# Kernel optimization log

Hardware: AMD Instinct MI355X
Metric: run time of the kernel (lower is better)

The kernel has to match this reference:

```python
import jax, jax.numpy as jnp
import numpy as np

D_MODEL = 512
HEADS = 8
HEAD_DIM = D_MODEL // HEADS
LN_EPS = 1e-5


def _rel_shift(pos_score):
    # pos_score: [B, H, T, P] with P = 2T-1
    B, H, T, P = pos_score.shape
    padded = jnp.pad(pos_score, ((0, 0), (0, 0), (0, 0), (1, 0)))  # [B,H,T,P+1]
    shifted = padded.reshape(B, H, P + 1, T)[:, :, 1:, :].reshape(B, H, T, P)
    return shifted[:, :, :, : P // 2 + 1]  # [B,H,T,T]


def setup_inputs() -> dict:
    key = jax.random.key(0)
    ks = jax.random.split(key, 16)
    B, T = 16, 512
    P = 2 * T - 1
    s = 1.0 / np.sqrt(D_MODEL)
    inp = {
        "x": jax.random.normal(ks[0], (B, T, D_MODEL), jnp.float32),
        "pos_emb": jax.random.normal(ks[1], (B, P, D_MODEL), jnp.float32),
        "ln_g": jnp.ones((D_MODEL,), jnp.float32),
        "ln_b": jnp.zeros((D_MODEL,), jnp.float32),
        "Wq": jax.random.normal(ks[2], (D_MODEL, D_MODEL), jnp.float32) * s,
        "bq": jnp.zeros((D_MODEL,), jnp.float32),
        "Wk": jax.random.normal(ks[3], (D_MODEL, D_MODEL), jnp.float32) * s,
        "bk": jnp.zeros((D_MODEL,), jnp.float32),
        "Wv": jax.random.normal(ks[4], (D_MODEL, D_MODEL), jnp.float32) * s,
        "bv": jnp.zeros((D_MODEL,), jnp.float32),
        "Wp": jax.random.normal(ks[5], (D_MODEL, D_MODEL), jnp.float32) * s,
        "bp": jnp.zeros((D_MODEL,), jnp.float32),
        "content_bias": jax.random.normal(ks[6], (HEADS, HEAD_DIM), jnp.float32) * 0.05,
        "position_bias": jax.random.normal(ks[7], (HEADS, HEAD_DIM), jnp.float32) * 0.05,
        "Wo": jax.random.normal(ks[8], (D_MODEL, D_MODEL), jnp.float32) * s,
        "bo": jnp.zeros((D_MODEL,), jnp.float32),
    }
    return inp


def reference(x, pos_emb, ln_g, ln_b, Wq, bq, Wk, bk, Wv, bv, Wp, bp,
              content_bias, position_bias, Wo, bo):
    B, T, D = x.shape
    H, hd = HEADS, HEAD_DIM

    # LayerNorm over last dim
    mu = jnp.mean(x, axis=-1, keepdims=True)
    var = jnp.var(x, axis=-1, keepdims=True)
    xn = (x - mu) / jnp.sqrt(var + LN_EPS) * ln_g + ln_b

    q = (xn @ Wq.T + bq).reshape(B, T, H, hd)                 # [B,T,H,hd]
    k = (xn @ Wk.T + bk).reshape(B, T, H, hd)                 # [B,T,H,hd]
    v = (xn @ Wv.T + bv).reshape(B, T, H, hd)                 # [B,T,H,hd]
    p = (pos_emb @ Wp.T + bp).reshape(B, -1, H, hd)           # [B,P,H,hd]

    content_score = jnp.einsum('bshd,bthd->bhst', q + content_bias, k)   # [B,H,T,T]
    pos_score = jnp.einsum('bshd,bphd->bhsp', q + position_bias, p)      # [B,H,T,P]
    pos_score = _rel_shift(pos_score)                                    # [B,H,T,T]

    scores = (content_score + pos_score) / jnp.sqrt(jnp.asarray(hd, x.dtype))
    w = jax.nn.softmax(scores, axis=-1)
    ctx = jnp.einsum('bhst,bthd->bshd', w, v).reshape(B, T, D)
    return ctx @ Wo.T + bo
```

## Files before the change

kernel.cpp:

```cpp
#include <hip/hip_runtime.h>
#include <cstdio>
#include <cstdint>


typedef short s16x8 __attribute__((ext_vector_type(8)));
typedef float f32x4 __attribute__((ext_vector_type(4)));
typedef unsigned short u16x4 __attribute__((ext_vector_type(4)));

#define CSCALE 0.1803368801111204f

#if __has_builtin(__builtin_amdgcn_exp2f)
#define EXP2(x) __builtin_amdgcn_exp2f(x)
#else
#define EXP2(x) exp2f(x)
#endif

__device__ __forceinline__ unsigned short f2bf(float f) {
  unsigned int u = __builtin_bit_cast(unsigned int, f);
  unsigned int r = (u + 0x7FFFu + ((u >> 16) & 1u)) >> 16;
  return (unsigned short)r;
}
__device__ __forceinline__ float bf2f(unsigned short h) {
  unsigned int u = ((unsigned int)h) << 16;
  return __builtin_bit_cast(float, u);
}

__device__ __forceinline__ void g2l16(const void* g, void* l) {
  __builtin_amdgcn_global_load_lds(
      (const __attribute__((address_space(1))) void*)g,
      (__attribute__((address_space(3))) void*)l, 16, 0, 0);
}

__global__ __launch_bounds__(256) void megaprep(
    const float* __restrict__ x, const float* __restrict__ g,
    const float* __restrict__ bb, unsigned short* __restrict__ xh,
    const float* __restrict__ pe, unsigned short* __restrict__ ped,
    const float* __restrict__ Wq, const float* __restrict__ Wk,
    const float* __restrict__ Wp, const float* __restrict__ Wv,
    const float* __restrict__ Wo, const float* __restrict__ bq,
    const float* __restrict__ bk, unsigned short* __restrict__ wqk,
    unsigned short* __restrict__ wpm, unsigned short* __restrict__ wvm,
    unsigned short* __restrict__ wom, float* __restrict__ bqk) {
  __shared__ float red[8];
  const int bid = blockIdx.x, tid = threadIdx.x;
  if (bid < 8192) {
    const int wave = tid >> 6, lane = tid & 63;
    const float* xr = x + (size_t)bid * 512;
    float v0 = xr[tid], v1 = xr[tid + 256];
    float s = v0 + v1, ss = v0 * v0 + v1 * v1;
#pragma unroll
    for (int d = 1; d < 64; d <<= 1) {
      s += __shfl_xor(s, d, 64);
      ss += __shfl_xor(ss, d, 64);
    }
    if (lane == 0) { red[wave] = s; red[4 + wave] = ss; }
    __syncthreads();
    s = red[0] + red[1] + red[2] + red[3];
    ss = red[4] + red[5] + red[6] + red[7];
    const float mu = s * (1.0f / 512.0f);
    const float var = ss * (1.0f / 512.0f) - mu * mu;
    const float rstd = rsqrtf(var + 1e-5f);
#pragma unroll
    for (int i = 0; i < 2; i++) {
      int d = tid + i * 256;
      float v = (i == 0) ? v0 : v1;
      float xn = (v - mu) * rstd * g[d] + bb[d];
      xh[(size_t)bid * 512 + d] = f2bf(xn);
    }
  } else if (bid < 16384) {
    int e0 = (bid - 8192) * 1024 + tid * 4;
    u16x4 o = {0, 0, 0, 0};
    if (e0 < 16368 * 512) {
      float4 v = *(const float4*)(pe + e0);
      o[0] = f2bf(v.x); o[1] = f2bf(v.y); o[2] = f2bf(v.z); o[3] = f2bf(v.w);
    }
    *(u16x4*)(ped + e0) = o;
  } else {
    int idx = (bid - 16384) * 1024 + tid * 4;
    int region = idx >> 18, off = idx & 262143;
    const float* src = (region == 0)   ? Wq
                       : (region == 1) ? Wk
                       : (region == 2) ? Wp
                       : (region == 3) ? Wv
                                       : Wo;
    float4 w = *(const float4*)(src + off);
    u16x4 hv;
    hv[0] = f2bf(w.x); hv[1] = f2bf(w.y); hv[2] = f2bf(w.z); hv[3] = f2bf(w.w);
    unsigned short* dst = (region == 0)   ? wqk
                          : (region == 1) ? wqk + 262144
                          : (region == 2) ? wpm
                          : (region == 3) ? wvm
                                          : wom;
    *(u16x4*)(dst + off) = hv;
    if (idx < 1024) {
#pragma unroll
      for (int j = 0; j < 4; j++) {
        int ii = idx + j;
        bqk[ii] = (ii < 512) ? bq[ii] : bk[ii - 512];
      }
    }
  }
}

__device__ __forceinline__ void gemm128_body(
    unsigned short* sm, int mode, int arow0, int m0e, int n0,
    const unsigned short* __restrict__ A, const unsigned short* __restrict__ B,
    const float* __restrict__ bias, void* __restrict__ O1, void* __restrict__ O2,
    void* __restrict__ O3, const float* __restrict__ cbv,
    const float* __restrict__ pbv) {
  unsigned short* bA = sm;
  unsigned short* bB = sm + 4096;
  const int tid = threadIdx.x, lane = tid & 63, wave = tid >> 6;
  const int wr = (wave >> 1) * 64, wc = (wave & 1) * 64;
  const int fr = lane & 15, hi2 = lane >> 4;
  const int l15 = lane & 15, lq = lane >> 4;

  f32x4 fz = {0.f, 0.f, 0.f, 0.f};
  f32x4 acc[4][4];
#pragma unroll
  for (int i = 0; i < 4; i++)
#pragma unroll
    for (int j = 0; j < 4; j++) acc[i][j] = fz;

  const unsigned short* gA0 = A + (size_t)(arow0 + wave * 32 + l15) * 512 + lq * 8;
  const unsigned short* gA1 = gA0 + 16 * 512;
  const unsigned short* gB0 = B + (size_t)(n0 + wave * 32 + l15) * 512 + lq * 8;
  const unsigned short* gB1 = gB0 + 16 * 512;
  char* dA0 = (char*)bA + wave * 2048;
  char* dA1 = dA0 + 1024;
  char* dB0 = (char*)bB + wave * 2048;
  char* dB1 = dB0 + 1024;
  const int atile = 4 * (wave >> 1), btile = 4 * (wave & 1);

  for (int k0 = 0; k0 < 512; k0 += 32) {
    __syncthreads();
    g2l16(gA0 + k0, dA0);
    g2l16(gA1 + k0, dA1);
    g2l16(gB0 + k0, dB0);
    g2l16(gB1 + k0, dB1);
    __syncthreads();
    s16x8 af[4], bf[4];
#pragma unroll
    for (int mt = 0; mt < 4; ++mt)
      af[mt] = *(const s16x8*)&bA[(atile + mt) * 512 + lane * 8];
#pragma unroll
    for (int nt = 0; nt < 4; ++nt)
      bf[nt] = *(const s16x8*)&bB[(btile + nt) * 512 + lane * 8];
#pragma unroll
    for (int mt = 0; mt < 4; ++mt)
#pragma unroll
      for (int nt = 0; nt < 4; ++nt)
        acc[mt][nt] = __builtin_amdgcn_mfma_f32_16x16x32_bf16(
            af[mt], bf[nt], acc[mt][nt], 0, 0, 0);
  }
#pragma unroll
  for (int nt = 0; nt < 4; ++nt) {
    int col = n0 + wc + nt * 16 + fr;
    float bval = bias[col];
#pragma unroll
    for (int mt = 0; mt < 4; ++mt) {
      int rowb_l = wr + mt * 16 + hi2 * 4;
      if (mode == 0) {
#pragma unroll
        for (int r = 0; r < 4; ++r)
          ((float*)O1)[(size_t)(m0e + rowb_l + r) * 512 + col] =
              acc[mt][nt][r] + bval;
      } else if (mode == 1) {
        int b = m0e >> 10, u0 = m0e & 1023;
        int h = col >> 6, cc = col & 63;
        size_t cbase = (size_t)(b * 8 + h) * 64 * 1024 + (cc >> 5) * 512 +
                       ((cc & 31) >> 3) * 128 + (cc & 7);
#pragma unroll
        for (int r = 0; r < 4; ++r) {
          int u = u0 + rowb_l + r;
          float val = (u >= 1023) ? 0.f : (acc[mt][nt][r] + bval);
          ((unsigned short*)O1)[cbase + (size_t)(u >> 4) * 1024 + (u & 15) * 8] =
              f2bf(val);
        }
      } else if (mode == 2) {
        int row = m0e + rowb_l;
        int b = row >> 9, s15 = row & 15, s16i = (row & 511) >> 4;
        if (col < 512) {
          int h = col >> 6, cc = col & 63;
          size_t idx = ((size_t)(b * 8 + h) * 32 + s16i) * 1024 +
                       (cc >> 5) * 512 + ((cc & 31) >> 3) * 128 + (cc & 7);
#pragma unroll
          for (int r = 0; r < 4; ++r) {
            float val = acc[mt][nt][r] + bval;
            ((unsigned short*)O1)[idx + (s15 + r) * 8] =
                f2bf((val + cbv[col]) * CSCALE);
            ((unsigned short*)O2)[idx + (s15 + r) * 8] =
                f2bf((val + pbv[col]) * CSCALE);
          }
        } else {
          int c2 = col - 512, h = c2 >> 6, cc = c2 & 63;
          size_t idx = ((size_t)(b * 8 + h) * 32 + s16i) * 1024 +
                       (cc >> 5) * 512 + ((cc & 31) >> 3) * 128 + (cc & 7);
#pragma unroll
          for (int r = 0; r < 4; ++r)
            ((unsigned short*)O3)[idx + (s15 + r) * 8] =
                f2bf(acc[mt][nt][r] + bval);
        }
      } else {
        int rowb = m0e + rowb_l;
        int b = rowb >> 9, t = rowb & 511;
        int h = col >> 6, d = col & 63;
        size_t idx = ((size_t)((b * 8 + h) * 4 + (d >> 4)) * 16 + (t >> 5)) * 512 +
                     ((t & 31) >> 3) * 128 + (d & 15) * 8 + (t & 7);
        u16x4 hv;
#pragma unroll
        for (int r = 0; r < 4; ++r) hv[r] = f2bf(acc[mt][nt][r] + bval);
        *(u16x4*)((unsigned short*)O1 + idx) = hv;
      }
    }
  }
}

__global__ __launch_bounds__(256) void proj_all(
    const unsigned short* __restrict__ xn_hi, const unsigned short* __restrict__ pe_hi,
    const unsigned short* __restrict__ wqk, const unsigned short* __restrict__ wpm,
    const unsigned short* __restrict__ wvm, const float* __restrict__ bqk,
    const float* __restrict__ bp, const float* __restrict__ bv,
    const float* __restrict__ cbv, const float* __restrict__ pbv,
    unsigned short* __restrict__ qc, unsigned short* __restrict__ qp,
    unsigned short* __restrict__ kb, unsigned short* __restrict__ pbuf,
    unsigned short* __restrict__ vth) {
  __shared__ __align__(16) unsigned short sm[8192];
  const int id = blockIdx.x;
  if (id < 512) {
    int m0 = (id >> 3) * 128, n0 = (id & 7) * 128;
    gemm128_body(sm, 2, m0, m0, n0, xn_hi, wqk, bqk, qc, qp, kb, cbv, pbv);
  } else if (id < 1024) {
    int l = id - 512;
    int y = l >> 2, n0 = (l & 3) * 128;
    int b = y >> 3, mt8 = y & 7;
    gemm128_body(sm, 1, b * 1023 + mt8 * 128, b * 1024 + mt8 * 128, n0, pe_hi,
                 wpm, bp, pbuf, nullptr, nullptr, nullptr, nullptr);
  } else {
    int l = id - 1024;
    int m0 = (l >> 2) * 128, n0 = (l & 3) * 128;
    gemm128_body(sm, 3, m0, m0, n0, xn_hi, wvm, bv, vth, nullptr, nullptr,
                 nullptr, nullptr);
  }
}

__global__ __launch_bounds__(256) void out_gemm(
    const unsigned short* __restrict__ ctx, const unsigned short* __restrict__ wom,
    const float* __restrict__ bo, float* __restrict__ out) {
  __shared__ __align__(16) unsigned short sm[8192];
  const int id = blockIdx.x;
  int m0 = (id >> 2) * 128, n0 = (id & 3) * 128;
  gemm128_body(sm, 0, m0, m0, n0, ctx, wom, bo, out, nullptr, nullptr,
               nullptr, nullptr);
}

__global__ __launch_bounds__(256) void flash_attn(
    const unsigned short* __restrict__ qc, const unsigned short* __restrict__ qp,
    const unsigned short* __restrict__ kb, const unsigned short* __restrict__ pm,
    const unsigned short* __restrict__ vth, unsigned short* __restrict__ ctx) {
  const int id = blockIdx.x;
  const int bh = id & 127, b = bh >> 3, h = bh & 7;
  const int s_blk = id >> 7;
  const int tid = threadIdx.x, wave = tid >> 6, lane = tid & 63;
  const int fr = lane & 15, hi2 = lane >> 4, fc = hi2 * 8;
  const int s0w = s_blk * 64 + wave * 16;
  const int crow = hi2 * 4;

  __shared__ __align__(16) unsigned short Ph_s[4][16][40];
  unsigned short(*Phw)[40] = Ph_s[wave];

  int srcl[4];
#pragma unroll
  for (int r = 0; r < 4; ++r) srcl[r] = (hi2 << 4) | ((fr - (crow + r) - 1) & 15);

  const size_t qtb = ((size_t)(b * 8 + h) * 32 + (s0w >> 4)) * 1024 + lane * 8;
  s16x8 aqc0 = *(const s16x8*)(qc + qtb);
  s16x8 aqc1 = *(const s16x8*)(qc + qtb + 512);
  s16x8 aqp0 = *(const s16x8*)(qp + qtb);
  s16x8 aqp1 = *(const s16x8*)(qp + qtb + 512);

  const unsigned short* kpk = kb + (size_t)(b * 8 + h) * 32 * 1024 + lane * 8;
  const unsigned short* ppk = pm + (size_t)(b * 8 + h) * 64 * 1024 + lane * 8;
  const unsigned short* vhk = vth + (size_t)(b * 8 + h) * 64 * 512 + lane * 8;

  f32x4 fz = {0.f, 0.f, 0.f, 0.f};
  f32x4 Oacc[4] = {fz, fz, fz, fz};
  float lsum[4] = {0.f, 0.f, 0.f, 0.f};

  for (int step = 0; step < 16; ++step) {
    const int t0 = step * 32;
    const int u0w = t0 - s0w + 496;
    const int kt = t0 >> 4, ut = u0w >> 4, vt = t0 >> 5;
    f32x4 sc[2] = {fz, fz};
#pragma unroll
    for (int nt = 0; nt < 2; ++nt) {
      const unsigned short* kr = kpk + (size_t)(kt + nt) * 1024;
      s16x8 b0 = *(const s16x8*)kr;
      s16x8 b1 = *(const s16x8*)(kr + 512);
      sc[nt] = __builtin_amdgcn_mfma_f32_16x16x32_bf16(aqc0, b0, sc[nt], 0, 0, 0);
      sc[nt] = __builtin_amdgcn_mfma_f32_16x16x32_bf16(aqc1, b1, sc[nt], 0, 0, 0);
    }
    f32x4 sp[3];
#pragma unroll
    for (int nt = 0; nt < 3; ++nt) {
      const unsigned short* pr = ppk + (size_t)(ut + nt) * 1024;
      s16x8 b0 = *(const s16x8*)pr;
      s16x8 b1 = *(const s16x8*)(pr + 512);
      f32x4 t = fz;
      t = __builtin_amdgcn_mfma_f32_16x16x32_bf16(aqp0, b0, t, 0, 0, 0);
      t = __builtin_amdgcn_mfma_f32_16x16x32_bf16(aqp1, b1, t, 0, 0, 0);
      sp[nt] = t;
    }
    float sj[3][4];
#pragma unroll
    for (int j = 0; j < 3; ++j)
#pragma unroll
      for (int r = 0; r < 4; ++r) sj[j][r] = __shfl(sp[j][r], srcl[r], 64);
#pragma unroll
    for (int nt = 0; nt < 2; ++nt) {
      int tc = nt * 16 + fr;
#pragma unroll
      for (int r = 0; r < 4; ++r) {
        float pos = (fr <= crow + r) ? sj[nt][r] : sj[nt + 1][r];
        float e = EXP2(sc[nt][r] + pos);
        lsum[r] += e;
        Phw[crow + r][tc] = f2bf(e);
      }
    }
    s16x8 ah = *(const s16x8*)&Phw[fr][fc];
#pragma unroll
    for (int nt = 0; nt < 4; ++nt) {
      s16x8 bh = *(const s16x8*)(vhk + (size_t)(nt * 16 + vt) * 512);
      Oacc[nt] = __builtin_amdgcn_mfma_f32_16x16x32_bf16(ah, bh, Oacc[nt], 0, 0, 0);
    }
  }
#pragma unroll
  for (int d = 1; d < 16; d <<= 1)
#pragma unroll
    for (int r = 0; r < 4; ++r) lsum[r] += __shfl_xor(lsum[r], d, 64);
#pragma unroll
  for (int nt = 0; nt < 4; ++nt)
#pragma unroll
    for (int r = 0; r < 4; ++r) {
      float o = Oacc[nt][r] / lsum[r];
      size_t idx =
          (size_t)(b * 512 + s0w + crow + r) * 512 + h * 64 + nt * 16 + fr;
      ctx[idx] = f2bf(o);
    }
}

extern "C" void kernel_launch(void* const* d_in, const int* in_sizes, int n_in,
                              void* d_out, int out_size, void* d_ws,
                              size_t ws_size, hipStream_t stream) {
  const float* x = (const float*)d_in[0];
  const float* pe = (const float*)d_in[1];
  const float* ln_g = (const float*)d_in[2];
  const float* ln_b = (const float*)d_in[3];
  const float* Wq = (const float*)d_in[4];
  const float* bq = (const float*)d_in[5];
  const float* Wk = (const float*)d_in[6];
  const float* bk = (const float*)d_in[7];
  const float* Wv = (const float*)d_in[8];
  const float* bv = (const float*)d_in[9];
  const float* Wp = (const float*)d_in[10];
  const float* bp = (const float*)d_in[11];
  const float* cb = (const float*)d_in[12];
  const float* pb = (const float*)d_in[13];
  const float* Wo = (const float*)d_in[14];
  const float* bo = (const float*)d_in[15];
  float* out = (float*)d_out;

  char* ws = (char*)d_ws;
  size_t off = 0;
  auto alloc = [&](size_t bytes) -> char* {
    char* ptr = ws + off;
    off = (off + bytes + 255) & ~(size_t)255;
    return ptr;
  };
  unsigned short* xn_hi = (unsigned short*)alloc((size_t)8192 * 512 * 2);
  unsigned short* ctx = xn_hi;
  unsigned short* pe_hi = (unsigned short*)alloc((size_t)16384 * 512 * 2);
  unsigned short* vt_hi = (unsigned short*)alloc((size_t)8192 * 512 * 2);
  unsigned short* wqk = (unsigned short*)alloc((size_t)1024 * 512 * 2);
  unsigned short* wpm = (unsigned short*)alloc((size_t)512 * 512 * 2);
  unsigned short* wvm = (unsigned short*)alloc((size_t)512 * 512 * 2);
  unsigned short* wom = (unsigned short*)alloc((size_t)512 * 512 * 2);
  float* bqk = (float*)alloc(1024 * 4);
  unsigned short* qc = (unsigned short*)alloc((size_t)8192 * 512 * 2);
  unsigned short* qp = (unsigned short*)alloc((size_t)8192 * 512 * 2);
  unsigned short* kbuf = (unsigned short*)alloc((size_t)8192 * 512 * 2);
  unsigned short* pbuf = (unsigned short*)alloc((size_t)16384 * 512 * 2);

  if (ws_size < off) {
    fprintf(stderr, "kernel_launch: ws too small (need %zu, have %zu)\n", off,
            ws_size);
    return;
  }

  megaprep<<<17664, 256, 0, stream>>>(x, ln_g, ln_b, xn_hi, pe, pe_hi, Wq, Wk,
                                      Wp, Wv, Wo, bq, bk, wqk, wpm, wvm, wom,
                                      bqk);
  proj_all<<<1280, 256, 0, stream>>>(xn_hi, pe_hi, wqk, wpm, wvm, bqk, bp, bv,
                                     cb, pb, qc, qp, kbuf, pbuf, vt_hi);
  flash_attn<<<1024, 256, 0, stream>>>(qc, qp, kbuf, pbuf, vt_hi, ctx);
  out_gemm<<<256, 256, 0, stream>>>(ctx, wom, bo, out);
}
```

Before: 232.9 us.

## Pre-pack GEMM operands into MFMA fragment layout and load directly without LDS

The prep kernel and attention output now write activations, positional embeddings and weights in a packed 16-row by 32-col fragment layout. This lets the projection and output GEMMs load MFMA operands straight from global memory per wave, with no LDS staging and no block barriers. Tiles shrink from 128x128 per block to 64x64 per wave. This removes shared-memory round trips and syncs, but gives up operand reuse across waves, so global and L2 traffic rises and the scattered packed writes in prep add cost.

```diff
diff --git a/kernel.cpp b/kernel.cpp
--- a/kernel.cpp
+++ b/kernel.cpp
@@ -24,17 +24,15 @@
   unsigned int u = ((unsigned int)h) << 16;
   return __builtin_bit_cast(float, u);
 }
-
-__device__ __forceinline__ void g2l16(const void* g, void* l) {
-  __builtin_amdgcn_global_load_lds(
-      (const __attribute__((address_space(1))) void*)g,
-      (__attribute__((address_space(3))) void*)l, 16, 0, 0);
+__device__ __forceinline__ size_t pk(int row, int col) {
+  return (size_t)(row >> 4) * 8192 + (col >> 5) * 512 + ((col >> 3) & 3) * 128 +
+         (row & 15) * 8 + (col & 7);
 }
 
 __global__ __launch_bounds__(256) void megaprep(
     const float* __restrict__ x, const float* __restrict__ g,
-    const float* __restrict__ bb, unsigned short* __restrict__ xh,
-    const float* __restrict__ pe, unsigned short* __restrict__ ped,
+    const float* __restrict__ bb, unsigned short* __restrict__ xpk,
+    const float* __restrict__ pe, unsigned short* __restrict__ pepk,
     const float* __restrict__ Wq, const float* __restrict__ Wk,
     const float* __restrict__ Wp, const float* __restrict__ Wv,
     const float* __restrict__ Wo, const float* __restrict__ bq,
@@ -65,16 +63,18 @@
       int d = tid + i * 256;
       float v = (i == 0) ? v0 : v1;
       float xn = (v - mu) * rstd * g[d] + bb[d];
-      xh[(size_t)bid * 512 + d] = f2bf(xn);
+      xpk[pk(bid, d)] = f2bf(xn);
     }
   } else if (bid < 16384) {
-    int e0 = (bid - 8192) * 1024 + tid * 4;
+    int e = (bid - 8192) * 1024 + tid * 4;
+    int r = e >> 9, c = e & 511;
+    int b = r >> 10, u = r & 1023;
     u16x4 o = {0, 0, 0, 0};
-    if (e0 < 16368 * 512) {
-      float4 v = *(const float4*)(pe + e0);
+    if (u < 1023) {
+      float4 v = *(const float4*)(pe + (size_t)(b * 1023 + u) * 512 + c);
       o[0] = f2bf(v.x); o[1] = f2bf(v.y); o[2] = f2bf(v.z); o[3] = f2bf(v.w);
     }
-    *(u16x4*)(ped + e0) = o;
+    *(u16x4*)(pepk + (size_t)b * 524288 + pk(u, c)) = o;
   } else {
     int idx = (bid - 16384) * 1024 + tid * 4;
     int region = idx >> 18, off = idx & 262143;
@@ -86,12 +86,15 @@
     float4 w = *(const float4*)(src + off);
     u16x4 hv;
     hv[0] = f2bf(w.x); hv[1] = f2bf(w.y); hv[2] = f2bf(w.z); hv[3] = f2bf(w.w);
-    unsigned short* dst = (region == 0)   ? wqk
-                          : (region == 1) ? wqk + 262144
-                          : (region == 2) ? wpm
-                          : (region == 3) ? wvm
-                                          : wom;
-    *(u16x4*)(dst + off) = hv;
+    int n = off >> 9, k = off & 511;
+    unsigned short* dst;
+    int nrow = n;
+    if (region == 0) { dst = wqk; }
+    else if (region == 1) { dst = wqk; nrow = n + 512; }
+    else if (region == 2) { dst = wpm; }
+    else if (region == 3) { dst = wvm; }
+    else { dst = wom; }
+    *(u16x4*)(dst + pk(nrow, k)) = hv;
     if (idx < 1024) {
 #pragma unroll
       for (int j = 0; j < 4; j++) {
@@ -102,50 +105,20 @@
   }
 }
 
-__device__ __forceinline__ void gemm128_body(
-    unsigned short* sm, int mode, int arow0, int m0e, int n0,
-    const unsigned short* __restrict__ A, const unsigned short* __restrict__ B,
-    const float* __restrict__ bias, void* __restrict__ O1, void* __restrict__ O2,
-    void* __restrict__ O3, const float* __restrict__ cbv,
-    const float* __restrict__ pbv) {
-  unsigned short* bA = sm;
-  unsigned short* bB = sm + 4096;
-  const int tid = threadIdx.x, lane = tid & 63, wave = tid >> 6;
-  const int wr = (wave >> 1) * 64, wc = (wave & 1) * 64;
-  const int fr = lane & 15, hi2 = lane >> 4;
-  const int l15 = lane & 15, lq = lane >> 4;
-
-  f32x4 fz = {0.f, 0.f, 0.f, 0.f};
-  f32x4 acc[4][4];
-#pragma unroll
-  for (int i = 0; i < 4; i++)
-#pragma unroll
-    for (int j = 0; j < 4; j++) acc[i][j] = fz;
-
-  const unsigned short* gA0 = A + (size_t)(arow0 + wave * 32 + l15) * 512 + lq * 8;
-  const unsigned short* gA1 = gA0 + 16 * 512;
-  const unsigned short* gB0 = B + (size_t)(n0 + wave * 32 + l15) * 512 + lq * 8;
-  const unsigned short* gB1 = gB0 + 16 * 512;
-  char* dA0 = (char*)bA + wave * 2048;
-  char* dA1 = dA0 + 1024;
-  char* dB0 = (char*)bB + wave * 2048;
-  char* dB1 = dB0 + 1024;
-  const int atile = 4 * (wave >> 1), btile = 4 * (wave & 1);
-
-  for (int k0 = 0; k0 < 512; k0 += 32) {
-    __syncthreads();
-    g2l16(gA0 + k0, dA0);
-    g2l16(gA1 + k0, dA1);
-    g2l16(gB0 + k0, dB0);
-    g2l16(gB1 + k0, dB1);
-    __syncthreads();
+__device__ __forceinline__ void gemm64_direct(
+    const unsigned short* __restrict__ Apk, const unsigned short* __restrict__ Bpk,
+    int mstrip0, int nstrip0, int lane, f32x4 acc[4][4]) {
+  const unsigned short* ab = Apk + (size_t)mstrip0 * 8192 + lane * 8;
+  const unsigned short* bb = Bpk + (size_t)nstrip0 * 8192 + lane * 8;
+#pragma unroll 4
+  for (int kc = 0; kc < 16; ++kc) {
     s16x8 af[4], bf[4];
 #pragma unroll
     for (int mt = 0; mt < 4; ++mt)
-      af[mt] = *(const s16x8*)&bA[(atile + mt) * 512 + lane * 8];
+      af[mt] = *(const s16x8*)(ab + (size_t)mt * 8192 + kc * 512);
 #pragma unroll
     for (int nt = 0; nt < 4; ++nt)
-      bf[nt] = *(const s16x8*)&bB[(btile + nt) * 512 + lane * 8];
+      bf[nt] = *(const s16x8*)(bb + (size_t)nt * 8192 + kc * 512);
 #pragma unroll
     for (int mt = 0; mt < 4; ++mt)
 #pragma unroll
@@ -153,71 +126,10 @@
         acc[mt][nt] = __builtin_amdgcn_mfma_f32_16x16x32_bf16(
             af[mt], bf[nt], acc[mt][nt], 0, 0, 0);
   }
-#pragma unroll
-  for (int nt = 0; nt < 4; ++nt) {
-    int col = n0 + wc + nt * 16 + fr;
-    float bval = bias[col];
-#pragma unroll
-    for (int mt = 0; mt < 4; ++mt) {
-      int rowb_l = wr + mt * 16 + hi2 * 4;
-      if (mode == 0) {
-#pragma unroll
-        for (int r = 0; r < 4; ++r)
-          ((float*)O1)[(size_t)(m0e + rowb_l + r) * 512 + col] =
-              acc[mt][nt][r] + bval;
-      } else if (mode == 1) {
-        int b = m0e >> 10, u0 = m0e & 1023;
-        int h = col >> 6, cc = col & 63;
-        size_t cbase = (size_t)(b * 8 + h) * 64 * 1024 + (cc >> 5) * 512 +
-                       ((cc & 31) >> 3) * 128 + (cc & 7);
-#pragma unroll
-        for (int r = 0; r < 4; ++r) {
-          int u = u0 + rowb_l + r;
-          float val = (u >= 1023) ? 0.f : (acc[mt][nt][r] + bval);
-          ((unsigned short*)O1)[cbase + (size_t)(u >> 4) * 1024 + (u & 15) * 8] =
-              f2bf(val);
-        }
-      } else if (mode == 2) {
-        int row = m0e + rowb_l;
-        int b = row >> 9, s15 = row & 15, s16i = (row & 511) >> 4;
-        if (col < 512) {
-          int h = col >> 6, cc = col & 63;
-          size_t idx = ((size_t)(b * 8 + h) * 32 + s16i) * 1024 +
-                       (cc >> 5) * 512 + ((cc & 31) >> 3) * 128 + (cc & 7);
-#pragma unroll
-          for (int r = 0; r < 4; ++r) {
-            float val = acc[mt][nt][r] + bval;
-            ((unsigned short*)O1)[idx + (s15 + r) * 8] =
-                f2bf((val + cbv[col]) * CSCALE);
-            ((unsigned short*)O2)[idx + (s15 + r) * 8] =
-                f2bf((val + pbv[col]) * CSCALE);
-          }
-        } else {
-          int c2 = col - 512, h = c2 >> 6, cc = c2 & 63;
-          size_t idx = ((size_t)(b * 8 + h) * 32 + s16i) * 1024 +
-                       (cc >> 5) * 512 + ((cc & 31) >> 3) * 128 + (cc & 7);
-#pragma unroll
-          for (int r = 0; r < 4; ++r)
-            ((unsigned short*)O3)[idx + (s15 + r) * 8] =
-                f2bf(acc[mt][nt][r] + bval);
-        }
-      } else {
-        int rowb = m0e + rowb_l;
-        int b = rowb >> 9, t = rowb & 511;
-        int h = col >> 6, d = col & 63;
-        size_t idx = ((size_t)((b * 8 + h) * 4 + (d >> 4)) * 16 + (t >> 5)) * 512 +
-                     ((t & 31) >> 3) * 128 + (d & 15) * 8 + (t & 7);
-        u16x4 hv;
-#pragma unroll
-        for (int r = 0; r < 4; ++r) hv[r] = f2bf(acc[mt][nt][r] + bval);
-        *(u16x4*)((unsigned short*)O1 + idx) = hv;
-      }
-    }
-  }
 }
 
 __global__ __launch_bounds__(256) void proj_all(
-    const unsigned short* __restrict__ xn_hi, const unsigned short* __restrict__ pe_hi,
+    const unsigned short* __restrict__ xpk, const unsigned short* __restrict__ pepk,
     const unsigned short* __restrict__ wqk, const unsigned short* __restrict__ wpm,
     const unsigned short* __restrict__ wvm, const float* __restrict__ bqk,
     const float* __restrict__ bp, const float* __restrict__ bv,
@@ -225,39 +137,133 @@
     unsigned short* __restrict__ qc, unsigned short* __restrict__ qp,
     unsigned short* __restrict__ kb, unsigned short* __restrict__ pbuf,
     unsigned short* __restrict__ vth) {
-  __shared__ __align__(16) unsigned short sm[8192];
-  const int id = blockIdx.x;
-  if (id < 512) {
-    int m0 = (id >> 3) * 128, n0 = (id & 7) * 128;
-    gemm128_body(sm, 2, m0, m0, n0, xn_hi, wqk, bqk, qc, qp, kb, cbv, pbv);
-  } else if (id < 1024) {
-    int l = id - 512;
-    int y = l >> 2, n0 = (l & 3) * 128;
-    int b = y >> 3, mt8 = y & 7;
-    gemm128_body(sm, 1, b * 1023 + mt8 * 128, b * 1024 + mt8 * 128, n0, pe_hi,
-                 wpm, bp, pbuf, nullptr, nullptr, nullptr, nullptr);
+  const int tid = threadIdx.x, lane = tid & 63, wave = tid >> 6;
+  const int w = blockIdx.x * 4 + wave;
+  const int fr = lane & 15, hi2 = lane >> 4;
+  f32x4 fz = {0.f, 0.f, 0.f, 0.f};
+  f32x4 acc[4][4];
+#pragma unroll
+  for (int i = 0; i < 4; i++)
+#pragma unroll
+    for (int j = 0; j < 4; j++) acc[i][j] = fz;
+
+  if (w < 2048) {
+    int m_t = w >> 4, n_t = w & 15;
+    gemm64_direct(xpk, wqk, m_t * 4, n_t * 4, lane, acc);
+    int m0 = m_t * 64, n0 = n_t * 64;
+#pragma unroll
+    for (int nt = 0; nt < 4; ++nt) {
+      int col = n0 + nt * 16 + fr;
+      float bval = bqk[col];
+#pragma unroll
+      for (int mt = 0; mt < 4; ++mt) {
+        int row = m0 + mt * 16 + hi2 * 4;
+        int b = row >> 9, s15 = row & 15, s16i = (row & 511) >> 4;
+        if (col < 512) {
+          int h = col >> 6, cc = col & 63;
+          size_t idx = ((size_t)(b * 8 + h) * 32 + s16i) * 1024 +
+                       (cc >> 5) * 512 + ((cc & 31) >> 3) * 128 + (cc & 7);
+          float cbc = cbv[col], pbc = pbv[col];
+#pragma unroll
+          for (int r = 0; r < 4; ++r) {
+            float val = acc[mt][nt][r] + bval;
+            qc[idx + (s15 + r) * 8] = f2bf((val + cbc) * CSCALE);
+            qp[idx + (s15 + r) * 8] = f2bf((val + pbc) * CSCALE);
+          }
+        } else {
+          int c2 = col - 512, h = c2 >> 6, cc = c2 & 63;
+          size_t idx = ((size_t)(b * 8 + h) * 32 + s16i) * 1024 +
+                       (cc >> 5) * 512 + ((cc & 31) >> 3) * 128 + (cc & 7);
+#pragma unroll
+          for (int r = 0; r < 4; ++r)
+            kb[idx + (s15 + r) * 8] = f2bf(acc[mt][nt][r] + bval);
+        }
+      }
+    }
+  } else if (w < 4096) {
+    int w2 = w - 2048;
+    int m_t = w2 >> 3, n_t = w2 & 7;
+    int bb_ = m_t >> 4;
+    gemm64_direct(pepk + (size_t)bb_ * 524288, wpm, (m_t & 15) * 4, n_t * 4,
+                  lane, acc);
+    int m0e = m_t * 64, n0 = n_t * 64;
+    int b = m0e >> 10, u0 = m0e & 1023;
+#pragma unroll
+    for (int nt = 0; nt < 4; ++nt) {
+      int col = n0 + nt * 16 + fr;
+      float bval = bp[col];
+      int h = col >> 6, cc = col & 63;
+      size_t cbase = (size_t)(b * 8 + h) * 64 * 1024 + (cc >> 5) * 512 +
+                     ((cc & 31) >> 3) * 128 + (cc & 7);
+#pragma unroll
+      for (int mt = 0; mt < 4; ++mt) {
+        int ub = u0 + mt * 16 + hi2 * 4;
+#pragma unroll
+        for (int r = 0; r < 4; ++r) {
+          int u = ub + r;
+          float val = (u >= 1023) ? 0.f : (acc[mt][nt][r] + bval);
+          pbuf[cbase + (size_t)(u >> 4) * 1024 + (u & 15) * 8] = f2bf(val);
+        }
+      }
+    }
   } else {
-    int l = id - 1024;
-    int m0 = (l >> 2) * 128, n0 = (l & 3) * 128;
-    gemm128_body(sm, 3, m0, m0, n0, xn_hi, wvm, bv, vth, nullptr, nullptr,
-                 nullptr, nullptr);
+    int w3 = w - 4096;
+    int m_t = w3 >> 3, n_t = w3 & 7;
+    gemm64_direct(xpk, wvm, m_t * 4, n_t * 4, lane, acc);
+    int m0 = m_t * 64, n0 = n_t * 64;
+#pragma unroll
+    for (int nt = 0; nt < 4; ++nt) {
+      int col = n0 + nt * 16 + fr;
+      float bval = bv[col];
+      int h = col >> 6, d = col & 63;
+#pragma unroll
+      for (int mt = 0; mt < 4; ++mt) {
+        int rowb = m0 + mt * 16 + hi2 * 4;
+        int b = rowb >> 9, t = rowb & 511;
+        size_t idx = ((size_t)((b * 8 + h) * 4 + (d >> 4)) * 16 + (t >> 5)) * 512 +
+                     ((t & 31) >> 3) * 128 + (d & 15) * 8 + (t & 7);
+        u16x4 hv;
+#pragma unroll
+        for (int r = 0; r < 4; ++r) hv[r] = f2bf(acc[mt][nt][r] + bval);
+        *(u16x4*)(vth + idx) = hv;
+      }
+    }
   }
 }
 
 __global__ __launch_bounds__(256) void out_gemm(
-    const unsigned short* __restrict__ ctx, const unsigned short* __restrict__ wom,
+    const unsigned short* __restrict__ ctxpk, const unsigned short* __restrict__ wom,
     const float* __restrict__ bo, float* __restrict__ out) {
-  __shared__ __align__(16) unsigned short sm[8192];
-  const int id = blockIdx.x;
-  int m0 = (id >> 2) * 128, n0 = (id & 3) * 128;
-  gemm128_body(sm, 0, m0, m0, n0, ctx, wom, bo, out, nullptr, nullptr,
-               nullptr, nullptr);
+  const int tid = threadIdx.x, lane = tid & 63, wave = tid >> 6;
+  const int w = blockIdx.x * 4 + wave;
+  const int fr = lane & 15, hi2 = lane >> 4;
+  int m_t = w >> 3, n_t = w & 7;
+  f32x4 fz = {0.f, 0.f, 0.f, 0.f};
+  f32x4 acc[4][4];
+#pragma unroll
+  for (int i = 0; i < 4; i++)
+#pragma unroll
+    for (int j = 0; j < 4; j++) acc[i][j] = fz;
+  gemm64_direct(ctxpk, wom, m_t * 4, n_t * 4, lane, acc);
+  int m0 = m_t * 64, n0 = n_t * 64;
+#pragma unroll
+  for (int nt = 0; nt < 4; ++nt) {
+    int col = n0 + nt * 16 + fr;
+    float bval = bo[col];
+#pragma unroll
+    for (int mt = 0; mt < 4; ++mt) {
+      int row = m0 + mt * 16 + hi2 * 4;
+#pragma unroll
+      for (int r = 0; r < 4; ++r)
+        out[(size_t)(row + r) * 512 + col] = acc[mt][nt][r] + bval;
+    }
+  }
 }
 
 __global__ __launch_bounds__(256) void flash_attn(
     const unsigned short* __restrict__ qc, const unsigned short* __restrict__ qp,
     const unsigned short* __restrict__ kb, const unsigned short* __restrict__ pm,
-    const unsigned short* __restrict__ vth, unsigned short* __restrict__ ctx) {
+    const unsigned short* __restrict__ vth, unsigned short* __restrict__ ctxpk) {
   const int id = blockIdx.x;
   const int bh = id & 127, b = bh >> 3, h = bh & 7;
   const int s_blk = id >> 7;
@@ -343,9 +349,9 @@
 #pragma unroll
     for (int r = 0; r < 4; ++r) {
       float o = Oacc[nt][r] / lsum[r];
-      size_t idx =
-          (size_t)(b * 512 + s0w + crow + r) * 512 + h * 64 + nt * 16 + fr;
-      ctx[idx] = f2bf(o);
+      int row = b * 512 + s0w + crow + r;
+      int col = h * 64 + nt * 16 + fr;
+      ctxpk[pk(row, col)] = f2bf(o);
     }
 }
 
@@ -377,9 +383,9 @@
     off = (off + bytes + 255) & ~(size_t)255;
     return ptr;
   };
-  unsigned short* xn_hi = (unsigned short*)alloc((size_t)8192 * 512 * 2);
-  unsigned short* ctx = xn_hi;
-  unsigned short* pe_hi = (unsigned short*)alloc((size_t)16384 * 512 * 2);
+  unsigned short* xpk = (unsigned short*)alloc((size_t)8192 * 512 * 2);
+  unsigned short* ctxpk = xpk;
+  unsigned short* pepk = (unsigned short*)alloc((size_t)16384 * 512 * 2);
   unsigned short* vt_hi = (unsigned short*)alloc((size_t)8192 * 512 * 2);
   unsigned short* wqk = (unsigned short*)alloc((size_t)1024 * 512 * 2);
   unsigned short* wpm = (unsigned short*)alloc((size_t)512 * 512 * 2);
@@ -397,11 +403,11 @@
     return;
   }
 
-  megaprep<<<17664, 256, 0, stream>>>(x, ln_g, ln_b, xn_hi, pe, pe_hi, Wq, Wk,
+  megaprep<<<17664, 256, 0, stream>>>(x, ln_g, ln_b, xpk, pe, pepk, Wq, Wk,
                                       Wp, Wv, Wo, bq, bk, wqk, wpm, wvm, wom,
                                       bqk);
-  proj_all<<<1280, 256, 0, stream>>>(xn_hi, pe_hi, wqk, wpm, wvm, bqk, bp, bv,
+  proj_all<<<1280, 256, 0, stream>>>(xpk, pepk, wqk, wpm, wvm, bqk, bp, bv,
                                      cb, pb, qc, qp, kbuf, pbuf, vt_hi);
-  flash_attn<<<1024, 256, 0, stream>>>(qc, qp, kbuf, pbuf, vt_hi, ctx);
-  out_gemm<<<256, 256, 0, stream>>>(ctx, wom, bo, out);
-}
+  flash_attn<<<1024, 256, 0, stream>>>(qc, qp, kbuf, pbuf, vt_hi, ctxpk);
+  out_gemm<<<256, 256, 0, stream>>>(ctxpk, wom, bo, out);
+}
```

Result: no change. 228.5 us (-1.9%).
